# Performance work log

Hardware: AMD Instinct MI355X
Metric: run time of the kernel (lower is better)

The kernel has to match this reference:

```python
import jax, jax.numpy as jnp
import numpy as np

B, S, D, H = 4, 2048, 768, 12
HD = D // H  # head_dim = 64


def setup_inputs() -> dict:
    key = jax.random.key(0)
    ks = jax.random.split(key, 5)
    scale = 0.02
    return {
        "x": jax.random.normal(ks[0], (B, S, D), dtype=jnp.float32),
        "wq": jax.random.normal(ks[1], (D, D), dtype=jnp.float32) * scale,
        "wk": jax.random.normal(ks[2], (D, D), dtype=jnp.float32) * scale,
        "wv": jax.random.normal(ks[3], (D, D), dtype=jnp.float32) * scale,
        "wo": jax.random.normal(ks[4], (D, D), dtype=jnp.float32) * scale,
        "bo": jnp.zeros((D,), dtype=jnp.float32),
    }


def reference(x, wq, wk, wv, wo, bo):
    b, s, d = x.shape
    # torch Linear: y = x @ W.T ; qkv_bias=False
    q = (x @ wq.T).reshape(b, s, H, HD).transpose(0, 2, 1, 3)  # [b,h,s,hd]
    k = (x @ wk.T).reshape(b, s, H, HD).transpose(0, 2, 1, 3)
    v = (x @ wv.T).reshape(b, s, H, HD).transpose(0, 2, 1, 3)
    scores = jnp.einsum("bhqd,bhkd->bhqk", q, k)  # full [b,h,s,s] score matrix
    causal = jnp.triu(jnp.ones((s, s), dtype=bool), k=1)
    scores = jnp.where(causal, -jnp.inf, scores)
    attn = jax.nn.softmax(scores / jnp.sqrt(jnp.float32(HD)), axis=-1)
    ctx = jnp.einsum("bhqk,bhkd->bhqd", attn, v)
    ctx = ctx.transpose(0, 2, 1, 3).reshape(b, s, d)
    return ctx @ wo.T + bo  # dropout is identity in eval mode
```

## Files before the change

### kernel.cpp

```cpp
#include <hip/hip_runtime.h>

#define H 12
#define S 2048
#define D 768
#define HD 64
#define BATCH 4
#define M_TOT (BATCH * S)

typedef __attribute__((ext_vector_type(8))) short bf16x8;
typedef __attribute__((ext_vector_type(4))) float f32x4;

__device__ __forceinline__ ushort f2bf(float f) {
  unsigned int x = __float_as_uint(f);
  x += 0x7fffu + ((x >> 16) & 1u);
  return (ushort)(x >> 16);
}

__device__ __forceinline__ uint cvt_pk_bf16(float lo, float hi) {
  uint r;
  asm("v_cvt_pk_bf16_f32 %0, %1, %2" : "=v"(r) : "v"(lo), "v"(hi));
  return r;
}

__device__ __forceinline__ void gload_lds16(const void* gsrc, void* lds) {
  __builtin_amdgcn_global_load_lds(
      (const __attribute__((address_space(1))) unsigned int*)gsrc,
      (__attribute__((address_space(3))) unsigned int*)lds, 16, 0, 0);
}

__global__ __launch_bounds__(256) void cast_all(
    const float* __restrict__ x, const float* __restrict__ wq,
    const float* __restrict__ wk, const float* __restrict__ wv,
    const float* __restrict__ wo, ushort* __restrict__ xb,
    ushort* __restrict__ wqb, ushort* __restrict__ wkb,
    ushort* __restrict__ wvb, ushort* __restrict__ wob) {
  const int NX = M_TOT * D / 4;
  const int NW = D * D / 4;
  int i = blockIdx.x * 256 + threadIdx.x;
  const float* src; ushort* dst; int off;
  if (i < NX) { src = x; dst = xb; off = i; }
  else {
    int j = i - NX; int w = j / NW; off = j - w * NW;
    src = (w == 0) ? wq : (w == 1) ? wk : (w == 2) ? wv : wo;
    dst = (w == 0) ? wqb : (w == 1) ? wkb : (w == 2) ? wvb : wob;
  }
  float4 f = reinterpret_cast<const float4*>(src)[off];
  ushort4 u;
  u.x = f2bf(f.x); u.y = f2bf(f.y); u.z = f2bf(f.z); u.w = f2bf(f.w);
  reinterpret_cast<ushort4*>(dst)[off] = u;
}

__global__ __launch_bounds__(256) void gemm_qkv(
    const ushort* __restrict__ xb, const ushort* __restrict__ wqb,
    const ushort* __restrict__ wkb, const ushort* __restrict__ wvb,
    ushort* __restrict__ qb, ushort* __restrict__ kb_,
    ushort* __restrict__ vtb, float qscale) {
  __shared__ ushort SM[3][8192];
  const int tid = threadIdx.x;
  const int lane = tid & 63, wid = tid >> 6;
  const int g = lane >> 4, li = lane & 15;
  const int wm = wid >> 1, wn = wid & 1;

  const int wg = blockIdx.x;
  const ushort *Ap, *Wp; ushort* ob; float osc; int m0, n0; bool vt;
  if (wg < 768) {
    vt = false;
    m0 = (wg & 63) * 128;
    const int y = wg >> 6;
    n0 = (y % 6) * 128;
    Ap = xb;
    if (y < 6) { Wp = wqb; ob = qb; osc = qscale; }
    else       { Wp = wkb; ob = kb_; osc = 1.0f; }
  } else {
    vt = true;
    const int t2 = wg - 768;
    m0 = (t2 % 6) * 128;
    n0 = (t2 / 6) * 128;
    Ap = wvb; Wp = xb; ob = vtb; osc = 1.0f;
  }

  const int rsub = lane >> 2;
  const int coff = (((lane & 3) ^ ((rsub >> 1) & 3)) << 3);

  auto stage = [&](int buf, int k0) {
#pragma unroll
    for (int rnd = 0; rnd < 2; ++rnd) {
      const int row0 = rnd * 64 + wid * 16;
      gload_lds16(&Ap[(size_t)(m0 + row0 + rsub) * 768 + k0 + coff], &SM[buf][row0 * 32]);
      gload_lds16(&Wp[(size_t)(n0 + row0 + rsub) * 768 + k0 + coff],
                  &SM[buf][4096 + row0 * 32]);
    }
  };

  f32x4 acc[4][4] = {};
  stage(0, 0);
  stage(1, 32);

  int cur = 0, pre = 2;
  for (int kt = 0; kt < 24; ++kt) {
    if (kt < 23) asm volatile("s_waitcnt vmcnt(4) lgkmcnt(0)" ::: "memory");
    else         asm volatile("s_waitcnt vmcnt(0) lgkmcnt(0)" ::: "memory");
    __builtin_amdgcn_s_barrier();
    if (kt + 2 < 24) stage(pre, (kt + 2) * 32);

    bf16x8 a[4], b[4];
#pragma unroll
    for (int i = 0; i < 4; ++i) {
      const int row = wm * 64 + i * 16 + li;
      a[i] = *reinterpret_cast<const bf16x8*>(
          &SM[cur][row * 32 + ((g ^ ((row >> 1) & 3)) << 3)]);
    }
#pragma unroll
    for (int j = 0; j < 4; ++j) {
      const int row = wn * 64 + j * 16 + li;
      b[j] = *reinterpret_cast<const bf16x8*>(
          &SM[cur][4096 + row * 32 + ((g ^ ((row >> 1) & 3)) << 3)]);
    }
    __builtin_amdgcn_s_setprio(1);
#pragma unroll
    for (int i = 0; i < 4; ++i)
#pragma unroll
      for (int j = 0; j < 4; ++j)
        acc[i][j] = __builtin_amdgcn_mfma_f32_16x16x32_bf16(a[i], b[j], acc[i][j], 0, 0, 0);
    __builtin_amdgcn_s_setprio(0);

    cur = (cur == 2) ? 0 : cur + 1;
    pre = (pre == 2) ? 0 : pre + 1;
  }

  __syncthreads();
  ushort* Cs = &SM[0][0];
#pragma unroll
  for (int i = 0; i < 4; ++i)
#pragma unroll
    for (int j = 0; j < 4; ++j)
#pragma unroll
      for (int r = 0; r < 4; ++r) {
        const int row = wm * 64 + i * 16 + g * 4 + r;
        const int col = wn * 64 + j * 16 + li;
        const int pc = ((((col >> 3) ^ (row & 7)) << 3) | (col & 7));
        Cs[row * 128 + pc] = f2bf(acc[i][j][r] * osc);
      }
  __syncthreads();

  const int row = tid >> 1, half = tid & 1;
  ushort* dst;
  if (!vt) {
    const int m = m0 + row;
    const int b_ = m >> 11, s_ = m & 2047;
    const int h_ = (n0 >> 6) + half;
    dst = &ob[(((size_t)b_ * H + h_) * S + s_) * HD];
  } else {
    const int mf = m0 + row;
    const int b_ = n0 >> 11;
    const int h_ = mf >> 6, hd_ = mf & 63;
    dst = &ob[(((size_t)b_ * H + h_) * HD + hd_) * S + (n0 & 2047) + half * 64];
  }
#pragma unroll
  for (int c8 = 0; c8 < 8; ++c8) {
    const int col = half * 64 + c8 * 8;
    const int chunk = (col >> 3) ^ (row & 7);
    bf16x8 vv = *reinterpret_cast<const bf16x8*>(&Cs[row * 128 + chunk * 8]);
    *reinterpret_cast<bf16x8*>(&dst[c8 * 8]) = vv;
  }
}

__global__ __launch_bounds__(256) void gemm_wo(const ushort* __restrict__ A,
                                               const ushort* __restrict__ W,
                                               float* __restrict__ out_f,
                                               const float* __restrict__ bias) {
  __shared__ ushort SM[3][6144];
  const int tid = threadIdx.x;
  const int lane = tid & 63, wid = tid >> 6;
  const int g = lane >> 4, li = lane & 15;
  const int wm = wid >> 1, wn = wid & 1;
  const int m0 = blockIdx.x * 64, n0 = blockIdx.y * 128;

  const int rsub = lane >> 2;
  const int coff = (((lane & 3) ^ ((rsub >> 1) & 3)) << 3);

  auto stage = [&](int buf, int k0) {
    gload_lds16(&A[(size_t)(m0 + wid * 16 + rsub) * 768 + k0 + coff],
                &SM[buf][wid * 16 * 32]);
#pragma unroll
    for (int rnd = 0; rnd < 2; ++rnd) {
      const int row0 = rnd * 64 + wid * 16;
      gload_lds16(&W[(size_t)(n0 + row0 + rsub) * 768 + k0 + coff],
                  &SM[buf][2048 + row0 * 32]);
    }
  };

  f32x4 acc[2][4] = {};
  stage(0, 0);
  stage(1, 32);

  int cur = 0, pre = 2;
  for (int kt = 0; kt < 24; ++kt) {
    if (kt < 23) asm volatile("s_waitcnt vmcnt(3) lgkmcnt(0)" ::: "memory");
    else         asm volatile("s_waitcnt vmcnt(0) lgkmcnt(0)" ::: "memory");
    __builtin_amdgcn_s_barrier();
    if (kt + 2 < 24) stage(pre, (kt + 2) * 32);

    bf16x8 a[2], b[4];
#pragma unroll
    for (int i = 0; i < 2; ++i) {
      const int row = wm * 32 + i * 16 + li;
      a[i] = *reinterpret_cast<const bf16x8*>(
          &SM[cur][row * 32 + ((g ^ ((row >> 1) & 3)) << 3)]);
    }
#pragma unroll
    for (int j = 0; j < 4; ++j) {
      const int row = wn * 64 + j * 16 + li;
      b[j] = *reinterpret_cast<const bf16x8*>(
          &SM[cur][2048 + row * 32 + ((g ^ ((row >> 1) & 3)) << 3)]);
    }
    __builtin_amdgcn_s_setprio(1);
#pragma unroll
    for (int i = 0; i < 2; ++i)
#pragma unroll
      for (int j = 0; j < 4; ++j)
        acc[i][j] = __builtin_amdgcn_mfma_f32_16x16x32_bf16(a[i], b[j], acc[i][j], 0, 0, 0);
    __builtin_amdgcn_s_setprio(0);

    cur = (cur == 2) ? 0 : cur + 1;
    pre = (pre == 2) ? 0 : pre + 1;
  }

#pragma unroll
  for (int i = 0; i < 2; ++i)
#pragma unroll
    for (int j = 0; j < 4; ++j)
#pragma unroll
      for (int r = 0; r < 4; ++r) {
        const int m = m0 + wm * 32 + i * 16 + g * 4 + r;
        const int n = n0 + wn * 64 + j * 16 + li;
        out_f[(size_t)m * 768 + n] = acc[i][j][r] + bias[n];
      }
}

__global__ __launch_bounds__(256) void attn_kernel(const ushort* __restrict__ Q,
                                                   const ushort* __restrict__ K,
                                                   const ushort* __restrict__ VT,
                                                   ushort* __restrict__ ctx) {
  __shared__ ushort Ks[2][64 * 64];
  __shared__ ushort Vts[2][64 * 64];
  __shared__ ushort Ps[4][32][72];

  const int tid = threadIdx.x;
  const int lane = tid & 63, wid = tid >> 6;
  const int g = lane >> 4, li = lane & 15;

  const int wg = blockIdx.x;
  const int xcd = wg & 7, t = wg >> 3;
  const int bh = xcd + 8 * (t >> 4);
  const int p = t & 15;
  const int qL = 64 * (31 - p), qS = 64 * p;

  const size_t base = (size_t)bh * S * HD;
  const size_t vtbase = (size_t)bh * HD * S;

  bf16x8 aq[2][2];
#pragma unroll
  for (int f = 0; f < 2; ++f) {
    const size_t qr = base + (size_t)((f ? qS : qL) + wid * 16 + li) * HD;
#pragma unroll
    for (int c = 0; c < 2; ++c)
      aq[f][c] = *reinterpret_cast<const bf16x8*>(&Q[qr + c * 32 + g * 8]);
  }

  f32x4 acc[2][4] = {};
  float lpart[2] = {0.f, 0.f};

  const int nkt = 32 - p;

  const int rsub = lane >> 3;
  const int c8e = (((lane & 7) ^ rsub) << 3);

  auto stage = [&](int buf, int k0) {
#pragma unroll
    for (int rnd = 0; rnd < 2; ++rnd) {
      const int row0 = rnd * 32 + wid * 8;
      gload_lds16(&K[base + (size_t)(k0 + row0 + rsub) * HD + c8e], &Ks[buf][row0 << 6]);
      gload_lds16(&VT[vtbase + (size_t)(row0 + rsub) * S + k0 + c8e], &Vts[buf][row0 << 6]);
    }
  };

  stage(0, 0);

  for (int kt = 0; kt < nkt; ++kt) {
    const int cur = kt & 1;
    const int k0 = kt * 64;
    const bool doS = (kt <= p);

    asm volatile("s_waitcnt vmcnt(0)" ::: "memory");
    __syncthreads();
    if (kt + 1 < nkt) stage(cur ^ 1, k0 + 64);

    f32x4 sc[2][4];
    __builtin_amdgcn_s_setprio(1);
#pragma unroll
    for (int ct = 0; ct < 4; ++ct) {
      const int row = ct * 16 + li, r7 = row & 7;
      const ushort* kr = &Ks[cur][row << 6];
      bf16x8 kb0 = *reinterpret_cast<const bf16x8*>(&kr[(g ^ r7) << 3]);
      bf16x8 kb1 = *reinterpret_cast<const bf16x8*>(&kr[((4 + g) ^ r7) << 3]);
      {
        f32x4 z = {};
        z = __builtin_amdgcn_mfma_f32_16x16x32_bf16(kb0, aq[0][0], z, 0, 0, 0);
        z = __builtin_amdgcn_mfma_f32_16x16x32_bf16(kb1, aq[0][1], z, 0, 0, 0);
        sc[0][ct] = z;
      }
      if (doS) {
        f32x4 z = {};
        z = __builtin_amdgcn_mfma_f32_16x16x32_bf16(kb0, aq[1][0], z, 0, 0, 0);
        z = __builtin_amdgcn_mfma_f32_16x16x32_bf16(kb1, aq[1][1], z, 0, 0, 0);
        sc[1][ct] = z;
      }
    }
    __builtin_amdgcn_s_setprio(0);

    if (kt == nkt - 1) {
      const int q = qL + wid * 16 + li;
#pragma unroll
      for (int ct = 0; ct < 4; ++ct)
#pragma unroll
        for (int r = 0; r < 4; ++r)
          if (k0 + ct * 16 + 4 * g + r > q) sc[0][ct][r] = -1e30f;
    }
    if (kt == p) {
      const int q = qS + wid * 16 + li;
#pragma unroll
      for (int ct = 0; ct < 4; ++ct)
#pragma unroll
        for (int r = 0; r < 4; ++r)
          if (k0 + ct * 16 + 4 * g + r > q) sc[1][ct][r] = -1e30f;
    }

#pragma unroll
    for (int f = 0; f < 2; ++f) {
      if (f == 1 && !doS) break;
#pragma unroll
      for (int ct = 0; ct < 4; ++ct) {
        float p0 = __builtin_amdgcn_exp2f(sc[f][ct][0]);
        float p1 = __builtin_amdgcn_exp2f(sc[f][ct][1]);
        float p2 = __builtin_amdgcn_exp2f(sc[f][ct][2]);
        float p3 = __builtin_amdgcn_exp2f(sc[f][ct][3]);
        lpart[f] += (p0 + p1) + (p2 + p3);
        uint2 pw;
        pw.x = cvt_pk_bf16(p0, p1);
        pw.y = cvt_pk_bf16(p2, p3);
        *reinterpret_cast<uint2*>(&Ps[wid][f * 16 + li][ct * 16 + 4 * g]) = pw;
      }
    }

    bf16x8 pa[2][2];
    pa[0][0] = *reinterpret_cast<const bf16x8*>(&Ps[wid][li][g * 8]);
    pa[0][1] = *reinterpret_cast<const bf16x8*>(&Ps[wid][li][32 + g * 8]);
    if (doS) {
      pa[1][0] = *reinterpret_cast<const bf16x8*>(&Ps[wid][16 + li][g * 8]);
      pa[1][1] = *reinterpret_cast<const bf16x8*>(&Ps[wid][16 + li][32 + g * 8]);
    }
    __builtin_amdgcn_s_setprio(1);
#pragma unroll
    for (int dt = 0; dt < 4; ++dt) {
      const int row = dt * 16 + li, r7 = row & 7;
      const ushort* vr = &Vts[cur][row << 6];
      bf16x8 vb0 = *reinterpret_cast<const bf16x8*>(&vr[(g ^ r7) << 3]);
      bf16x8 vb1 = *reinterpret_cast<const bf16x8*>(&vr[((4 + g) ^ r7) << 3]);
      acc[0][dt] = __builtin_amdgcn_mfma_f32_16x16x32_bf16(pa[0][0], vb0, acc[0][dt], 0, 0, 0);
      acc[0][dt] = __builtin_amdgcn_mfma_f32_16x16x32_bf16(pa[0][1], vb1, acc[0][dt], 0, 0, 0);
      if (doS) {
        acc[1][dt] = __builtin_amdgcn_mfma_f32_16x16x32_bf16(pa[1][0], vb0, acc[1][dt], 0, 0, 0);
        acc[1][dt] = __builtin_amdgcn_mfma_f32_16x16x32_bf16(pa[1][1], vb1, acc[1][dt], 0, 0, 0);
      }
    }
    __builtin_amdgcn_s_setprio(0);
  }

  const int b = bh / H, h = bh % H;
#pragma unroll
  for (int f = 0; f < 2; ++f) {
    float l = lpart[f];
    l += __shfl_xor(l, 16);
    l += __shfl_xor(l, 32);
#pragma unroll
    for (int r = 0; r < 4; ++r) {
      float inv = 1.0f / __shfl(l, 4 * g + r);
      const int s = (f ? qS : qL) + wid * 16 + 4 * g + r;
#pragma unroll
      for (int dt = 0; dt < 4; ++dt)
        ctx[((size_t)(b * S + s)) * D + h * HD + dt * 16 + li] =
            f2bf(acc[f][dt][r] * inv);
    }
  }
}

extern "C" void kernel_launch(void* const* d_in, const int* in_sizes, int n_in,
                              void* d_out, int out_size, void* d_ws, size_t ws_size,
                              hipStream_t stream) {
  (void)in_sizes; (void)n_in; (void)out_size; (void)ws_size;
  const float* x  = (const float*)d_in[0];
  const float* wq = (const float*)d_in[1];
  const float* wk = (const float*)d_in[2];
  const float* wv = (const float*)d_in[3];
  const float* wo = (const float*)d_in[4];
  const float* bo = (const float*)d_in[5];
  float* out = (float*)d_out;

  const size_t xn = (size_t)M_TOT * D;
  const size_t wn = (size_t)D * D;

  ushort* p = (ushort*)d_ws;
  ushort* x_bf  = p; p += xn;
  ushort* wq_bf = p; p += wn;
  ushort* wk_bf = p; p += wn;
  ushort* wv_bf = p; p += wn;
  ushort* wo_bf = p; p += wn;
  ushort* q_bf  = p; p += xn;
  ushort* k_bf  = p; p += xn;
  ushort* vt_bf = p; p += xn;
  ushort* ctx_bf = x_bf;

  cast_all<<<8448, 256, 0, stream>>>(x, wq, wk, wv, wo,
                                     x_bf, wq_bf, wk_bf, wv_bf, wo_bf);

  const float QSCALE = 0.125f * 1.44269504f;
  gemm_qkv<<<1152, 256, 0, stream>>>(x_bf, wq_bf, wk_bf, wv_bf,
                                     q_bf, k_bf, vt_bf, QSCALE);

  attn_kernel<<<768, 256, 0, stream>>>(q_bf, k_bf, vt_bf, ctx_bf);

  gemm_wo<<<dim3(128, 6), 256, 0, stream>>>(ctx_bf, wo_bf, out, bo);
}
```

Baseline: 132.3 us.

## Replace double-buffered direct-to-LDS K/V loads with register-staged single buffer

The attention kernel now prefetches the next K and V^T tiles into registers with ordinary global loads, then writes them into a single LDS buffer after a second barrier, instead of issuing direct-to-LDS loads into a double buffer. This halves the LDS used for K/V, which could allow more workgroups per CU, and drops the vmcnt(0) wait at the top of each iteration. In exchange it adds a second __syncthreads per iteration, extra VGPRs for the staged data, and explicit LDS store instructions.

```diff
diff --git a/kernel.cpp b/kernel.cpp
--- a/kernel.cpp
+++ b/kernel.cpp
@@ -242,8 +242,8 @@
                                                    const ushort* __restrict__ K,
                                                    const ushort* __restrict__ VT,
                                                    ushort* __restrict__ ctx) {
-  __shared__ ushort Ks[2][64 * 64];
-  __shared__ ushort Vts[2][64 * 64];
+  __shared__ ushort Ks[64 * 64];
+  __shared__ ushort Vts[64 * 64];
   __shared__ ushort Ps[4][32][72];
 
   const int tid = threadIdx.x;
@@ -274,34 +274,42 @@
   const int nkt = 32 - p;
 
   const int rsub = lane >> 3;
-  const int c8e = (((lane & 7) ^ rsub) << 3);
-
-  auto stage = [&](int buf, int k0) {
-#pragma unroll
-    for (int rnd = 0; rnd < 2; ++rnd) {
-      const int row0 = rnd * 32 + wid * 8;
-      gload_lds16(&K[base + (size_t)(k0 + row0 + rsub) * HD + c8e], &Ks[buf][row0 << 6]);
-      gload_lds16(&VT[vtbase + (size_t)(row0 + rsub) * S + k0 + c8e], &Vts[buf][row0 << 6]);
-    }
-  };
-
-  stage(0, 0);
+  const int c8 = (lane & 7) * 8;
+  const int wr = (((lane & 7) ^ rsub) << 3);
+  const int r0a = wid * 8 + rsub;
+  const int r0b = 32 + wid * 8 + rsub;
+
+  uint4 sk0, sk1, sv0, sv1;
+  sk0 = *reinterpret_cast<const uint4*>(&K[base + (size_t)r0a * HD + c8]);
+  sk1 = *reinterpret_cast<const uint4*>(&K[base + (size_t)r0b * HD + c8]);
+  sv0 = *reinterpret_cast<const uint4*>(&VT[vtbase + (size_t)r0a * S + c8]);
+  sv1 = *reinterpret_cast<const uint4*>(&VT[vtbase + (size_t)r0b * S + c8]);
+  *reinterpret_cast<uint4*>(&Ks[r0a * 64 + wr]) = sk0;
+  *reinterpret_cast<uint4*>(&Ks[r0b * 64 + wr]) = sk1;
+  *reinterpret_cast<uint4*>(&Vts[r0a * 64 + wr]) = sv0;
+  *reinterpret_cast<uint4*>(&Vts[r0b * 64 + wr]) = sv1;
 
   for (int kt = 0; kt < nkt; ++kt) {
-    const int cur = kt & 1;
     const int k0 = kt * 64;
     const bool doS = (kt <= p);
 
-    asm volatile("s_waitcnt vmcnt(0)" ::: "memory");
     __syncthreads();
-    if (kt + 1 < nkt) stage(cur ^ 1, k0 + 64);
+
+    if (kt + 1 < nkt) {
+      const int kn = k0 + 64;
+      sk0 = *reinterpret_cast<const uint4*>(&K[base + (size_t)(kn + r0a) * HD + c8]);
+      sk1 = *reinterpret_cast<const uint4*>(&K[base + (size_t)(kn + r0b) * HD + c8]);
+      sv0 = *reinterpret_cast<const uint4*>(&VT[vtbase + (size_t)r0a * S + kn + c8]);
+      sv1 = *reinterpret_cast<const uint4*>(&VT[vtbase + (size_t)r0b * S + kn + c8]);
+    }
+    __builtin_amdgcn_sched_barrier(0);
 
     f32x4 sc[2][4];
     __builtin_amdgcn_s_setprio(1);
 #pragma unroll
     for (int ct = 0; ct < 4; ++ct) {
       const int row = ct * 16 + li, r7 = row & 7;
-      const ushort* kr = &Ks[cur][row << 6];
+      const ushort* kr = &Ks[row << 6];
       bf16x8 kb0 = *reinterpret_cast<const bf16x8*>(&kr[(g ^ r7) << 3]);
       bf16x8 kb1 = *reinterpret_cast<const bf16x8*>(&kr[((4 + g) ^ r7) << 3]);
       {
@@ -364,7 +372,7 @@
 #pragma unroll
     for (int dt = 0; dt < 4; ++dt) {
       const int row = dt * 16 + li, r7 = row & 7;
-      const ushort* vr = &Vts[cur][row << 6];
+      const ushort* vr = &Vts[row << 6];
       bf16x8 vb0 = *reinterpret_cast<const bf16x8*>(&vr[(g ^ r7) << 3]);
       bf16x8 vb1 = *reinterpret_cast<const bf16x8*>(&vr[((4 + g) ^ r7) << 3]);
       acc[0][dt] = __builtin_amdgcn_mfma_f32_16x16x32_bf16(pa[0][0], vb0, acc[0][dt], 0, 0, 0);
@@ -375,6 +383,14 @@
       }
     }
     __builtin_amdgcn_s_setprio(0);
+
+    __syncthreads();
+    if (kt + 1 < nkt) {
+      *reinterpret_cast<uint4*>(&Ks[r0a * 64 + wr]) = sk0;
+      *reinterpret_cast<uint4*>(&Ks[r0b * 64 + wr]) = sk1;
+      *reinterpret_cast<uint4*>(&Vts[r0a * 64 + wr]) = sv0;
+      *reinterpret_cast<uint4*>(&Vts[r0b * 64 + wr]) = sv1;
+    }
   }
 
   const int b = bh / H, h = bh % H;
```

Measured after the change: 152.3 us. +15.1%, slower.
